# Kernel tuning notes

Hardware: AMD Instinct MI355X
Metric: run time of the kernel (lower is better)

Reference implementation:

```python
import jax, jax.numpy as jnp
import numpy as np

M_MARGIN = 0.25
GAMMA = 64.0
EPS = 1e-5


def _circle_loss_one_way(enc, dec):
    # enc, dec: [N, D]. Faithful to the torch rotate-concat construction:
    # cos_sim[j, k] = cosine(enc[j], dec[(j + k) % N]); column 0 is the positive.
    N = enc.shape[0]
    dot = enc @ dec.T                                   # [N, N]
    en = jnp.sqrt(jnp.sum(enc * enc, axis=1, keepdims=True))   # [N, 1]
    dn = jnp.sqrt(jnp.sum(dec * dec, axis=1, keepdims=True))   # [N, 1]
    S = dot / (en * dn.T + EPS)                         # [N, N] cosine sims
    r = jnp.arange(N)
    idx = (r[:, None] + r[None, :]) % N                 # [N, N] rolled column index
    cos_sim = jnp.take_along_axis(S, idx, axis=1)       # [N, N]
    sp = cos_sim[:, 0:1]                                # [N, 1] positives (diag of S)
    sn = cos_sim[:, 1:]                                 # [N, N-1] negatives
    ap = jnp.maximum(-jax.lax.stop_gradient(sp) + 1.0 + M_MARGIN, 0.0)
    an = jnp.maximum(jax.lax.stop_gradient(sn) + M_MARGIN, 0.0)
    delta_p = 1.0 - M_MARGIN
    delta_n = M_MARGIN
    logit_p = -ap * (sp - delta_p) * GAMMA              # [N, 1]
    logit_n = an * (sn - delta_n) * GAMMA               # [N, N-1]
    lse_n = jax.nn.logsumexp(logit_n, axis=0)           # [N-1]
    lse_p = jax.nn.logsumexp(logit_p, axis=0)           # [1] (cols of repeated sp are identical)
    return jax.nn.softplus(lse_n + lse_p)               # [N-1]


def reference(encoder_output, decoder_output):
    loss_a = _circle_loss_one_way(encoder_output, decoder_output)
    loss_b = _circle_loss_one_way(decoder_output, encoder_output)
    return jnp.mean((loss_a + loss_b) / 2.0)


def setup_inputs() -> dict:
    key = jax.random.key(0)
    k1, k2 = jax.random.split(key)
    N, D = 8192, 128
    return {
        "encoder_output": jax.random.normal(k1, (N, D), dtype=jnp.float32),
        "decoder_output": jax.random.normal(k2, (N, D), dtype=jnp.float32),
    }
```

## Files before the change

### kernel.cpp

```cpp
#include <hip/hip_runtime.h>
#include <hip/hip_bf16.h>

#define NN 8192

using f32x4 = __attribute__((ext_vector_type(4))) float;

#if __has_builtin(__builtin_amdgcn_exp2f)
#define EXP2(x) __builtin_amdgcn_exp2f(x)
#else
#define EXP2(x) __expf((x) * 0.69314718056f)
#endif

__device__ __forceinline__ void gl_lds16(const void* g, void* l) {
  __builtin_amdgcn_global_load_lds(
      (const __attribute__((address_space(1))) unsigned int*)(unsigned long long)g,
      (__attribute__((address_space(3))) unsigned int*)(unsigned int)(unsigned long long)l,
      16, 0, 0);
}

#if __has_builtin(__builtin_amdgcn_cvt_pk_fp8_f32)
__device__ __forceinline__ unsigned pk4_fp8(float x0, float x1, float x2, float x3) {
  unsigned w = (unsigned)__builtin_amdgcn_cvt_pk_fp8_f32(x0, x1, 0, false);
  w = (unsigned)__builtin_amdgcn_cvt_pk_fp8_f32(x2, x3, (int)w, true);
  return w;
}
#else
__device__ __forceinline__ unsigned f8_1(float f) {
  unsigned u = __float_as_uint(f);
  unsigned s = (u >> 24) & 0x80u;
  float a = fabsf(f);
  if (a < 0.015625f) {
    unsigned m = (unsigned)rintf(a * 512.0f);
    return s | (m > 7u ? 8u : m);
  }
  if (a > 448.0f) return s | 0x7Eu;
  unsigned au = u & 0x7FFFFFFFu;
  unsigned e = (au >> 23) - 127u + 7u;
  unsigned m23 = au & 0x7FFFFFu;
  unsigned m = m23 >> 20;
  unsigned rem = m23 & 0xFFFFFu;
  if (rem > 0x80000u || (rem == 0x80000u && (m & 1u))) {
    if (++m == 8u) { m = 0u; ++e; }
  }
  return s | (e << 3) | m;
}
__device__ __forceinline__ unsigned pk4_fp8(float x0, float x1, float x2, float x3) {
  return f8_1(x0) | (f8_1(x1) << 8) | (f8_1(x2) << 16) | (f8_1(x3) << 24);
}
#endif

__global__ __launch_bounds__(256) void k_prep(const float* __restrict__ enc,
                                              const float* __restrict__ dec,
                                              uint2* __restrict__ A8,
                                              uint2* __restrict__ B8,
                                              float* __restrict__ logit_p,
                                              float* __restrict__ bandsum,
                                              unsigned* __restrict__ counter) {
  const int t = threadIdx.x;
  const int l16 = t & 15;
  const int row = blockIdx.x * 16 + (t >> 4);
  const int tid = blockIdx.x * 256 + t;
  if (tid < 64 * 256) bandsum[tid] = 0.0f;
  if (tid == 64 * 256) *counter = 0u;

  const float4* e4 = reinterpret_cast<const float4*>(enc) + (size_t)row * 32 + l16 * 2;
  const float4* d4 = reinterpret_cast<const float4*>(dec) + (size_t)row * 32 + l16 * 2;
  float4 e0 = e4[0], e1 = e4[1];
  float4 d0 = d4[0], d1 = d4[1];

  float se = e0.x*e0.x + e0.y*e0.y + e0.z*e0.z + e0.w*e0.w
           + e1.x*e1.x + e1.y*e1.y + e1.z*e1.z + e1.w*e1.w;
  float sd = d0.x*d0.x + d0.y*d0.y + d0.z*d0.z + d0.w*d0.w
           + d1.x*d1.x + d1.y*d1.y + d1.z*d1.z + d1.w*d1.w;
  float sp = e0.x*d0.x + e0.y*d0.y + e0.z*d0.z + e0.w*d0.w
           + e1.x*d1.x + e1.y*d1.y + e1.z*d1.z + e1.w*d1.w;
#pragma unroll
  for (int off = 1; off < 16; off <<= 1) {
    se += __shfl_xor(se, off);
    sd += __shfl_xor(sd, off);
    sp += __shfl_xor(sp, off);
  }
  float ie = rsqrtf(se), id = rsqrtf(sd);

  uint2 ua, ub;
  ua.x = pk4_fp8(e0.x * ie, e0.y * ie, e0.z * ie, e0.w * ie);
  ua.y = pk4_fp8(e1.x * ie, e1.y * ie, e1.z * ie, e1.w * ie);
  ub.x = pk4_fp8(d0.x * id, d0.y * id, d0.z * id, d0.w * id);
  ub.y = pk4_fp8(d1.x * id, d1.y * id, d1.z * id, d1.w * id);
  A8[(size_t)row * 16 + l16] = ua;
  B8[(size_t)row * 16 + l16] = ub;

  if (l16 == 0) {
    float en = se * ie, dn = sd * id;
    float s  = sp / (en * dn + 1e-5f);
    logit_p[row] = -fmaxf(1.25f - s, 0.0f) * (s - 0.75f) * 64.0f;
  }
}

__global__ __launch_bounds__(256, 3) void k_main(const unsigned char* __restrict__ A,
                                                 const unsigned char* __restrict__ B,
                                                 float* __restrict__ bandsum,
                                                 const float* __restrict__ logit_p,
                                                 unsigned* __restrict__ counter,
                                                 float* __restrict__ out) {
  __shared__ __align__(16) unsigned char As[16384];
  __shared__ __align__(16) unsigned char Bs[16384];
  __shared__ float part[4][256];
  __shared__ unsigned lastFlag;

  const int t  = threadIdx.x;
  const int T  = blockIdx.x;
  const int sp = blockIdx.y;

#pragma unroll
  for (int q = 0; q < 4; ++q) part[q][t] = 0.0f;

  const int lane = t & 63;
  const int w = t >> 6, wrow = w >> 1, wcol = w & 1;
  const int l15 = lane & 15, quad = lane >> 4;
  const int x7 = l15 & 7;
  const int qh = quad >> 1, ql8 = (quad & 1) * 8;

  const int rl = t >> 3;
  const int lgoff = rl * 128 + ((t & 7) ^ (rl & 7)) * 16;
  const int lloff = t * 16;

  const char* Ab = (const char*)A;
  const char* Bb = (const char*)B;

  float dreg[28];
#pragma unroll
  for (int i = 0; i < 28; ++i) dreg[i] = 0.0f;

  const int arow = (wrow * 64 + l15) * 128;
  const int brow = (wcol * 64 + l15) * 128;

  {
    const int by = sp * 4;
    const int bx = (by + T) & 63;
    const char* Ag = Ab + (size_t)by * 16384 + lgoff;
    const char* Bg = Bb + (size_t)bx * 16384 + lgoff;
#pragma unroll
    for (int j = 0; j < 4; ++j) {
      gl_lds16(Ag + j * 4096, (char*)As + j * 4096 + lloff);
      gl_lds16(Bg + j * 4096, (char*)Bs + j * 4096 + lloff);
    }
  }
  __syncthreads();

  for (int it = 0; it < 4; ++it) {
    f32x4 acc[4][4];
    const f32x4 zv = {0.f, 0.f, 0.f, 0.f};
#pragma unroll
    for (int r = 0; r < 4; ++r)
#pragma unroll
      for (int c = 0; c < 4; ++c) acc[r][c] = zv;

#pragma unroll
    for (int ks = 0; ks < 4; ++ks) {
      long a[4], b[4];
      const int off = (((ks * 2 + qh) ^ x7) * 16) + ql8;
#pragma unroll
      for (int r = 0; r < 4; ++r)
        a[r] = *reinterpret_cast<const long*>((const char*)As + arow + r * 2048 + off);
#pragma unroll
      for (int c = 0; c < 4; ++c)
        b[c] = *reinterpret_cast<const long*>((const char*)Bs + brow + c * 2048 + off);
#pragma unroll
      for (int r = 0; r < 4; ++r)
#pragma unroll
        for (int c = 0; c < 4; ++c)
          acc[r][c] = __builtin_amdgcn_mfma_f32_16x16x32_fp8_fp8(a[r], b[c], acc[r][c], 0, 0, 0);
    }

    __syncthreads();

    if (it < 3) {
      const int by = sp * 4 + it + 1;
      const int bx = (by + T) & 63;
      const char* Ag = Ab + (size_t)by * 16384 + lgoff;
      const char* Bg = Bb + (size_t)bx * 16384 + lgoff;
#pragma unroll
      for (int j = 0; j < 4; ++j) {
        gl_lds16(Ag + j * 4096, (char*)As + j * 4096 + lloff);
        gl_lds16(Bg + j * 4096, (char*)Bs + j * 4096 + lloff);
      }
    }

#pragma unroll
    for (int dlt = -3; dlt <= 3; ++dlt) {
#pragma unroll
      for (int g = 0; g < 4; ++g) {
        float s = 0.0f;
#pragma unroll
        for (int r = 0; r < 4; ++r) {
          int c = r + dlt;
          if (c < 0 || c > 3) continue;
          float sn = acc[r][c][g];
          float an = fmaxf(sn + 0.25f, 0.0f);
          float u  = fmaf(sn, 92.332483f, -23.083121f);
          s += EXP2(an * u);
        }
        dreg[(dlt + 3) * 4 + g] += s;
      }
    }

    if (it < 3) __syncthreads();
  }

  const int  Qoff = (wcol - wrow) * 64 + 127;
  const int  v    = l15 - quad * 4;
  const bool leader = (quad == 0) || (l15 <= 3);
  const bool ok1 = (l15 <= 11) && (quad <= 2);
  const bool ok2 = (l15 <= 7)  && (quad <= 1);

#pragma unroll
  for (int dlt = -3; dlt <= 3; ++dlt) {
#pragma unroll
    for (int g = 0; g < 4; ++g) {
      float s = dreg[(dlt + 3) * 4 + g];
      float t1 = __shfl_down(s, 20); s += ok1 ? t1 : 0.0f;
      float t2 = __shfl_down(s, 40); s += ok2 ? t2 : 0.0f;
      int ld = Qoff + dlt * 16 - g + v;
      if (leader) unsafeAtomicAdd(&part[w][ld], s);
    }
  }
  __syncthreads();

  if (t < 255) {
    float vv = part[0][t] + part[1][t] + part[2][t] + part[3][t];
    unsafeAtomicAdd(&bandsum[T * 256 + t], vv);
  }

  __syncthreads();
  if (t == 0) lastFlag = (atomicAdd(counter, 1u) == 1023u) ? 1u : 0u;
  __syncthreads();
  if (!lastFlag) return;

  __threadfence();
  float* sm = part[0];

  float lp[32];
#pragma unroll
  for (int k = 0; k < 32; ++k) lp[k] = logit_p[t + 256 * k];

  float m = lp[0];
#pragma unroll
  for (int k = 1; k < 32; ++k) m = fmaxf(m, lp[k]);
#pragma unroll
  for (int off = 32; off; off >>= 1) m = fmaxf(m, __shfl_down(m, off));
  if (lane == 0) sm[w] = m;
  __syncthreads();
  m = fmaxf(fmaxf(sm[0], sm[1]), fmaxf(sm[2], sm[3]));
  __syncthreads();

  float s = 0.0f;
#pragma unroll
  for (int k = 0; k < 32; ++k) s += __expf(lp[k] - m);
#pragma unroll
  for (int off = 32; off; off >>= 1) s += __shfl_down(s, off);
  if (lane == 0) sm[w] = s;
  __syncthreads();
  s = sm[0] + sm[1] + sm[2] + sm[3];
  float lse_p = m + __logf(s);
  __syncthreads();

  const int o  = t & 127;
  const int hi = t >> 7;
  float bs1[32], bs2[32];
#pragma unroll
  for (int k = 0; k < 32; ++k) {
    int Ta = hi + 2 * k;
    bs1[k] = bandsum[Ta * 256 + o + 127];
    bs2[k] = o ? bandsum[((Ta + 1) & 63) * 256 + o - 1] : 0.0f;
  }
  float acc = 0.0f;
#pragma unroll
  for (int k = 0; k < 32; ++k) {
    if (t == 0 && k == 0) continue;
    float se = bs1[k] + bs2[k];
    float x = __logf(se) + lse_p;
    acc += fmaxf(x, 0.0f) + __logf(1.0f + __expf(-fabsf(x)));
  }
#pragma unroll
  for (int off = 32; off; off >>= 1) acc += __shfl_down(acc, off);
  if (lane == 0) sm[w] = acc;
  __syncthreads();
  if (t == 0) out[0] = (sm[0] + sm[1] + sm[2] + sm[3]) * (1.0f / 8191.0f);
}

extern "C" void kernel_launch(void* const* d_in, const int* in_sizes, int n_in,
                              void* d_out, int out_size, void* d_ws, size_t ws_size,
                              hipStream_t stream) {
  const float* enc = (const float*)d_in[0];
  const float* dec = (const float*)d_in[1];
  float* ws = (float*)d_ws;

  float*    logit_p = ws;
  float*    bandsum = ws + 8192;
  unsigned* counter = (unsigned*)(ws + 8192 + 16384);
  uint2*    A8      = (uint2*)(ws + 8192 + 16384 + 256);
  uint2*    B8      = (uint2*)((char*)A8 + 1048576);
  float*    out     = (float*)d_out;

  k_prep<<<NN / 16, 256, 0, stream>>>(enc, dec, A8, B8, logit_p, bandsum, counter);
  dim3 grid(64, 16);
  k_main<<<grid, 256, 0, stream>>>((const unsigned char*)A8, (const unsigned char*)B8,
                                   bandsum, logit_p, counter, out);
}
```

Before: 106.9 us.

## Store fp8 operands in MFMA fragment order and load directly from global

The prep kernel now writes normalized fp8 rows in a panel-major layout that matches the 16x16x32 MFMA fragment order. The main kernel drops the LDS staging buffers, async global-to-LDS copies and barriers, and each wave loads its A/B fragments straight from global memory as coalesced 8-byte loads. This removes LDS traffic and synchronization but gives up the prefetch overlap and makes every wave read its operands from L2/global with no shared reuse.

```diff
diff --git a/kernel.cpp b/kernel.cpp
--- a/kernel.cpp
+++ b/kernel.cpp
@@ -10,13 +10,6 @@
 #else
 #define EXP2(x) __expf((x) * 0.69314718056f)
 #endif
-
-__device__ __forceinline__ void gl_lds16(const void* g, void* l) {
-  __builtin_amdgcn_global_load_lds(
-      (const __attribute__((address_space(1))) unsigned int*)(unsigned long long)g,
-      (__attribute__((address_space(3))) unsigned int*)(unsigned int)(unsigned long long)l,
-      16, 0, 0);
-}
 
 #if __has_builtin(__builtin_amdgcn_cvt_pk_fp8_f32)
 __device__ __forceinline__ unsigned pk4_fp8(float x0, float x1, float x2, float x3) {
@@ -87,8 +80,11 @@
   ua.y = pk4_fp8(e1.x * ie, e1.y * ie, e1.z * ie, e1.w * ie);
   ub.x = pk4_fp8(d0.x * id, d0.y * id, d0.z * id, d0.w * id);
   ub.y = pk4_fp8(d1.x * id, d1.y * id, d1.z * id, d1.w * id);
-  A8[(size_t)row * 16 + l16] = ua;
-  B8[(size_t)row * 16 + l16] = ub;
+
+  const int panel = row >> 4;
+  const int dst = panel * 256 + (l16 >> 2) * 64 + (l16 & 3) * 16 + (row & 15);
+  A8[dst] = ua;
+  B8[dst] = ub;
 
   if (l16 == 0) {
     float en = se * ie, dn = sd * id;
@@ -103,8 +99,6 @@
                                                  const float* __restrict__ logit_p,
                                                  unsigned* __restrict__ counter,
                                                  float* __restrict__ out) {
-  __shared__ __align__(16) unsigned char As[16384];
-  __shared__ __align__(16) unsigned char Bs[16384];
   __shared__ float part[4][256];
   __shared__ unsigned lastFlag;
 
@@ -118,37 +112,17 @@
   const int lane = t & 63;
   const int w = t >> 6, wrow = w >> 1, wcol = w & 1;
   const int l15 = lane & 15, quad = lane >> 4;
-  const int x7 = l15 & 7;
-  const int qh = quad >> 1, ql8 = (quad & 1) * 8;
-
-  const int rl = t >> 3;
-  const int lgoff = rl * 128 + ((t & 7) ^ (rl & 7)) * 16;
-  const int lloff = t * 16;
-
-  const char* Ab = (const char*)A;
-  const char* Bb = (const char*)B;
 
   float dreg[28];
 #pragma unroll
   for (int i = 0; i < 28; ++i) dreg[i] = 0.0f;
 
-  const int arow = (wrow * 64 + l15) * 128;
-  const int brow = (wcol * 64 + l15) * 128;
-
-  {
-    const int by = sp * 4;
+  for (int it = 0; it < 4; ++it) {
+    const int by = sp * 4 + it;
     const int bx = (by + T) & 63;
-    const char* Ag = Ab + (size_t)by * 16384 + lgoff;
-    const char* Bg = Bb + (size_t)bx * 16384 + lgoff;
-#pragma unroll
-    for (int j = 0; j < 4; ++j) {
-      gl_lds16(Ag + j * 4096, (char*)As + j * 4096 + lloff);
-      gl_lds16(Bg + j * 4096, (char*)Bs + j * 4096 + lloff);
-    }
-  }
-  __syncthreads();
-
-  for (int it = 0; it < 4; ++it) {
+    const uint2* Af = (const uint2*)(A + (size_t)by * 16384 + wrow * 8192) + lane;
+    const uint2* Bf = (const uint2*)(B + (size_t)bx * 16384 + wcol * 8192) + lane;
+
     f32x4 acc[4][4];
     const f32x4 zv = {0.f, 0.f, 0.f, 0.f};
 #pragma unroll
@@ -159,32 +133,21 @@
 #pragma unroll
     for (int ks = 0; ks < 4; ++ks) {
       long a[4], b[4];
-      const int off = (((ks * 2 + qh) ^ x7) * 16) + ql8;
-#pragma unroll
-      for (int r = 0; r < 4; ++r)
-        a[r] = *reinterpret_cast<const long*>((const char*)As + arow + r * 2048 + off);
-#pragma unroll
-      for (int c = 0; c < 4; ++c)
-        b[c] = *reinterpret_cast<const long*>((const char*)Bs + brow + c * 2048 + off);
+#pragma unroll
+      for (int r = 0; r < 4; ++r) {
+        uint2 va = Af[r * 256 + ks * 64];
+        a[r] = (long)(((unsigned long long)va.y << 32) | va.x);
+      }
+#pragma unroll
+      for (int c = 0; c < 4; ++c) {
+        uint2 vb = Bf[c * 256 + ks * 64];
+        b[c] = (long)(((unsigned long long)vb.y << 32) | vb.x);
+      }
 #pragma unroll
       for (int r = 0; r < 4; ++r)
 #pragma unroll
         for (int c = 0; c < 4; ++c)
           acc[r][c] = __builtin_amdgcn_mfma_f32_16x16x32_fp8_fp8(a[r], b[c], acc[r][c], 0, 0, 0);
-    }
-
-    __syncthreads();
-
-    if (it < 3) {
-      const int by = sp * 4 + it + 1;
-      const int bx = (by + T) & 63;
-      const char* Ag = Ab + (size_t)by * 16384 + lgoff;
-      const char* Bg = Bb + (size_t)bx * 16384 + lgoff;
-#pragma unroll
-      for (int j = 0; j < 4; ++j) {
-        gl_lds16(Ag + j * 4096, (char*)As + j * 4096 + lloff);
-        gl_lds16(Bg + j * 4096, (char*)Bs + j * 4096 + lloff);
-      }
     }
 
 #pragma unroll
@@ -204,8 +167,6 @@
         dreg[(dlt + 3) * 4 + g] += s;
       }
     }
-
-    if (it < 3) __syncthreads();
   }
 
   const int  Qoff = (wcol - wrow) * 64 + 127;
```

Result: faster. 104.2 us (-2.5%).
